# Performance work log

Measured on AMD Instinct MI355X. Metric: run time of the kernel, lower is better.

## Reference

```python
import jax, jax.numpy as jnp
from jax import lax
import numpy as np

N, D, H, ENT = 32768, 16, 128, 50000


def setup_inputs() -> dict:
    key = jax.random.key(0)
    ks = jax.random.split(key, 10)
    s = 0.05  # weight scale to keep tanh/sigmoid in active range
    return {
        "ent_table": jax.random.normal(ks[0], (ENT, H), jnp.float32) * s,
        "op_table": jax.random.normal(ks[1], (5, H), jnp.float32) * s,
        "non_table": jax.random.normal(ks[2], (1, H), jnp.float32) * s,
        "Wm": jax.random.normal(ks[3], (H, 3 * H), jnp.float32) * s,
        "bm": jnp.zeros((H,), jnp.float32),
        "Wg": jax.random.normal(ks[4], (H, 3 * H), jnp.float32) * s,
        "bg": jnp.zeros((H,), jnp.float32),
        "ops_idx": jax.random.randint(ks[5], (N, D), 0, 4, jnp.int32),
        "ents_idx": jax.random.randint(ks[6], (N, D + 1), 0, ENT, jnp.int32),
        "left_idx": jax.random.randint(ks[7], (N,), 0, ENT, jnp.int32),
    }


def reference(ent_table, op_table, non_table, Wm, bm, Wg, bg, ops_idx, ents_idx, left_idx):
    # Merge module (dropout in eval mode = identity):
    #   tanh(Linear([node, t1, t2])) * sigmoid(Linear_g([node, t1, t2]))
    def merge(node, t1, t2):
        x = jnp.concatenate([node, t1, t2], axis=-1)  # [N, 3H]
        return jnp.tanh(x @ Wm.T + bm) * jax.nn.sigmoid(x @ Wg.T + bg)

    op_e = op_table[ops_idx]        # [N, D, H]
    ent_e = ent_table[ents_idx]     # [N, D+1, H]

    # Right-leaning prefix tree: acc starts at deepest entity, merge upward.
    acc0 = ent_e[:, -1]             # [N, H]
    # scan over depth, from innermost (i = D-1) to outermost (i = 0)
    xs = (jnp.flip(op_e, axis=1).transpose(1, 0, 2),          # [D, N, H]
          jnp.flip(ent_e[:, :-1], axis=1).transpose(1, 0, 2))  # [D, N, H]

    def step(acc, inp):
        o, e = inp
        return merge(o, e, acc), None

    acc, _ = lax.scan(step, acc0, xs)

    eq_e = jnp.broadcast_to(op_table[4], acc.shape)  # '=' embedding, [N, H]
    left_e = ent_table[left_idx]                     # [N, H]
    score = merge(eq_e, left_e, acc)                 # [N, H]

    # all_score = cat(per-formula scores, non_embed)  -> [N+1, H]
    return jnp.concatenate([score, non_table], axis=0)
```

## Files before the change

kernel.cpp:

```cpp
#include <hip/hip_runtime.h>
#include <hip/hip_bf16.h>
#include <hip/hip_fp16.h>

#define NROWS 32768
#define HH 128
#define ENTN 50000

typedef _Float16 f16x8 __attribute__((ext_vector_type(8)));
typedef __fp16 fp16x2 __attribute__((ext_vector_type(2)));
typedef float f32x4 __attribute__((ext_vector_type(4)));
typedef float f32x16 __attribute__((ext_vector_type(16)));

#define OFF_PEB 0
#define OFF_WF  25600000
#define OFF_PEF (OFF_WF + 65536)
#define OFF_POPK (OFF_PEF + 65536)

#define KM 2.8853901f
#define KG (-1.4426950f)
#define RSTR 272
#define HALF (32 * RSTR)

#if defined(__has_builtin)
#if __has_builtin(__builtin_amdgcn_exp2f)
#define FEXP2(x) __builtin_amdgcn_exp2f(x)
#endif
#endif
#ifndef FEXP2
__device__ __forceinline__ float __fexp2_asm(float x) {
    float r; asm("v_exp_f32 %0, %1" : "=v"(r) : "v"(x)); return r;
}
#define FEXP2(x) __fexp2_asm(x)
#endif

__device__ __forceinline__ unsigned pk2(float a, float b) {
    fp16x2 h = __builtin_amdgcn_cvt_pkrtz(a, b);
    unsigned u; __builtin_memcpy(&u, &h, 4); return u;
}
__device__ __forceinline__ unsigned pk2rtn(float a, float b) {
    _Float16 lo = (_Float16)a, hi = (_Float16)b;
    unsigned short ul, uh;
    __builtin_memcpy(&ul, &lo, 2); __builtin_memcpy(&uh, &hi, 2);
    return (unsigned)ul | ((unsigned)uh << 16);
}

__global__ void prep_kernel(const float* __restrict__ op_table,
                            const float* __restrict__ non_table,
                            const float* __restrict__ Wm, const float* __restrict__ bm,
                            const float* __restrict__ Wg, const float* __restrict__ bg,
                            char* __restrict__ ws, float* __restrict__ out) {
    int idx = blockIdx.x * blockDim.x + threadIdx.x;
    if (idx < 32768) {
        int e = idx;
        int jj = e & 7, l = (e >> 3) & 63, kt = (e >> 9) & 7, jb = e >> 12;
        int j = jb * 32 + (l & 31);
        int c = j >> 1, p = j & 1;
        int k = kt * 16 + (l >> 5) * 8 + jj;
        const float* Wrow = p ? (Wg + (size_t)c * 384) : (Wm + (size_t)c * 384);
        ((_Float16*)(ws + OFF_WF))[e] = (_Float16)(Wrow[256 + k] * (p ? KG : KM));
    } else if (idx < 65536) {
        int e = idx - 32768;
        int jj = e & 7, l = (e >> 3) & 63, kt = (e >> 9) & 3, jbf = e >> 11;
        int fr = l & 15;
        int j = (jbf >> 1) * 32 + 8 * (fr >> 2) + 4 * (jbf & 1) + (fr & 3);
        int c = j >> 1, p = j & 1;
        int k = kt * 32 + (l >> 4) * 8 + jj;
        const float* Wrow = p ? (Wg + (size_t)c * 384) : (Wm + (size_t)c * 384);
        ((_Float16*)(ws + OFF_PEF))[e] = (_Float16)Wrow[128 + k];
    } else if (idx < 66176) {
        int t2 = idx - 65536;
        int pr = t2 & 1, q = (t2 >> 1) & 3, h = (t2 >> 3) & 1, jb = (t2 >> 4) & 7, o = t2 >> 7;
        int j0 = jb * 32 + 8 * q + 4 * h + 2 * pr;
        int c = j0 >> 1;
        float sm = bm[c], sg = bg[c];
        const float* Wrm = Wm + (size_t)c * 384;
        const float* Wrg = Wg + (size_t)c * 384;
        for (int i = 0; i < 128; ++i) {
            float ov = op_table[o * HH + i];
            sm += ov * Wrm[i];
            sg += ov * Wrg[i];
        }
        ((unsigned*)(ws + OFF_POPK))[t2] = pk2rtn(sm * KM, sg * KG);
    } else if (idx < 66304) {
        int j = idx - 66176;
        out[(size_t)NROWS * HH + j] = non_table[j];
    }
}

__global__ __launch_bounds__(256, 4)
void pe_kernel(const float* __restrict__ ent_table, char* __restrict__ ws) {
    const f16x8* PEF = (const f16x8*)(ws + OFF_PEF);
    char* PEB = ws + OFF_PEB;
    int tid = threadIdx.x, w = tid >> 6, l = tid & 63, lr = l & 15, lg = (l >> 4) & 3;
    int e0 = blockIdx.x * 32;

    f16x8 WB[4][4];
    #pragma unroll
    for (int u = 0; u < 4; ++u)
        #pragma unroll
        for (int kt = 0; kt < 4; ++kt)
            WB[u][kt] = PEF[((4 * w + u) * 4 + kt) * 64 + l];

    f32x4 C[2][4];
    #pragma unroll
    for (int rt = 0; rt < 2; ++rt)
        #pragma unroll
        for (int u = 0; u < 4; ++u) C[rt][u] = (f32x4){0.f, 0.f, 0.f, 0.f};

    #pragma unroll
    for (int kt = 0; kt < 4; ++kt) {
        #pragma unroll
        for (int rt = 0; rt < 2; ++rt) {
            int e = e0 + rt * 16 + lr;
            if (e >= ENTN) e = ENTN - 1;
            const float4* s = (const float4*)(ent_table + (size_t)e * HH + kt * 32 + lg * 8);
            float4 v0 = s[0], v1 = s[1];
            unsigned u4[4] = {pk2(v0.x, v0.y), pk2(v0.z, v0.w),
                              pk2(v1.x, v1.y), pk2(v1.z, v1.w)};
            f16x8 A; __builtin_memcpy(&A, u4, 16);
            #pragma unroll
            for (int u = 0; u < 4; ++u)
                C[rt][u] = __builtin_amdgcn_mfma_f32_16x16x32_f16(WB[u][kt], A, C[rt][u], 0, 0, 0);
        }
    }
    #pragma unroll
    for (int rt = 0; rt < 2; ++rt) {
        int e = e0 + rt * 16 + lr;
        if (e < ENTN) {
            #pragma unroll
            for (int u = 0; u < 4; ++u) {
                int jb2 = 2 * w + (u >> 1);
                uint2 st;
                st.x = pk2(C[rt][u][0] * KM, C[rt][u][1] * KG);
                st.y = pk2(C[rt][u][2] * KM, C[rt][u][3] * KG);
                *(uint2*)(PEB + (size_t)e * 512 + jb2 * 64 + (u & 1) * 32 + lg * 8) = st;
            }
        }
    }
}

__global__ __launch_bounds__(512, 4)
void chain_kernel(const float* __restrict__ ent_table,
                  const int* __restrict__ ops_idx,
                  const int* __restrict__ ents_idx,
                  const int* __restrict__ left_idx,
                  const char* __restrict__ ws, float* __restrict__ out) {
    __shared__ char Abuf[2 * HALF];
    __shared__ unsigned eo[17 * 32];
    __shared__ unsigned popk[640];

    const char* PEBc = ws + OFF_PEB;
    const f16x8* WFp = (const f16x8*)(ws + OFF_WF);
    const unsigned* POPKg = (const unsigned*)(ws + OFF_POPK);

    int tid = threadIdx.x;
    int jb = tid >> 6, l = tid & 63, r = l & 31, h = l >> 5;
    int row0 = blockIdx.x * 32;

    for (int i = tid; i < 544; i += 512) {
        int t = i >> 5, rr = i & 31;
        unsigned e, o;
        if (t < 16) {
            e = ents_idx[(row0 + rr) * 17 + 15 - t];
            o = ops_idx[(row0 + rr) * 16 + 15 - t];
        } else {
            e = left_idx[row0 + rr];
            o = 4;
        }
        eo[i] = (e << 9) | o;
    }
    for (int i = tid; i < 640; i += 512) popk[i] = POPKg[i];

    f16x8 WH[8];
    #pragma unroll
    for (int kt = 0; kt < 8; ++kt)
        WH[kt] = WFp[(jb * 8 + kt) * 64 + l];

    {
        int rr = tid >> 4, sub = tid & 15;
        int e = ents_idx[(row0 + rr) * 17 + 16];
        const float4* src = (const float4*)(ent_table + (size_t)e * HH + sub * 8);
        float4 v0 = src[0], v1 = src[1];
        uint4 d;
        d.x = pk2(v0.x, v0.y); d.y = pk2(v0.z, v0.w);
        d.z = pk2(v1.x, v1.y); d.w = pk2(v1.z, v1.w);
        *(uint4*)(Abuf + rr * RSTR + sub * 16) = d;
    }
    __syncthreads();

    int rb = r * RSTR + h * 16;
    int wb = r * RSTR + jb * 32 + h * 4;
    const char* pebBase = PEBc + jb * 64 + h * 32;
    const char* popkB = (const char*)popk + jb * 64 + h * 32;
    const unsigned* eoB = eo + r;

    unsigned va = eoB[0];
    uint4 pa0 = *(const uint4*)(pebBase + (va & 0xFFFFFE00u));
    uint4 pa1 = *(const uint4*)(pebBase + (va & 0xFFFFFE00u) + 16);

#define DO_STEP(T, RD, WR, FINAL)                                               \
    {                                                                           \
        uint4 npa0, npa1; unsigned nva = 0;                                     \
        if (!(FINAL)) {                                                         \
            nva = eoB[((T) + 1) * 32];                                          \
            npa0 = *(const uint4*)(pebBase + (nva & 0xFFFFFE00u));              \
            npa1 = *(const uint4*)(pebBase + (nva & 0xFFFFFE00u) + 16);         \
        }                                                                       \
        const char* pq = popkB + (va & 7u) * 512;                               \
        uint4 po0 = *(const uint4*)(pq);                                        \
        uint4 po1 = *(const uint4*)(pq + 16);                                   \
        unsigned pe_u[8] = {pa0.x, pa0.y, pa0.z, pa0.w, pa1.x, pa1.y, pa1.z, pa1.w}; \
        unsigned po_u[8] = {po0.x, po0.y, po0.z, po0.w, po1.x, po1.y, po1.z, po1.w}; \
        f32x16 C;                                                               \
        _Pragma("unroll")                                                       \
        for (int q = 0; q < 4; ++q)                                             \
            _Pragma("unroll")                                                   \
            for (int pr = 0; pr < 2; ++pr) {                                    \
                int u = q * 2 + pr;                                             \
                __half2 sa = *(const __half2*)&pe_u[u];                         \
                __half2 sb = *(const __half2*)&po_u[u];                         \
                __half2 s = __hadd2(sa, sb);                                    \
                C[4 * q + 2 * pr] = __low2float(s);                             \
                C[4 * q + 2 * pr + 1] = __high2float(s);                        \
            }                                                                   \
        _Pragma("unroll")                                                       \
        for (int kt = 0; kt < 8; ++kt) {                                        \
            f16x8 A = *(const f16x8*)(Abuf + rb + (RD) + kt * 32);              \
            C = __builtin_amdgcn_mfma_f32_32x32x16_f16(WH[kt], A, C, 0, 0, 0);  \
        }                                                                       \
        _Pragma("unroll")                                                       \
        for (int q = 0; q < 4; ++q) {                                           \
            float ov[2];                                                        \
            _Pragma("unroll")                                                   \
            for (int pr = 0; pr < 2; ++pr) {                                    \
                float m = C[4 * q + 2 * pr];                                    \
                float g = C[4 * q + 2 * pr + 1];                                \
                float em = FEXP2(m), eg = FEXP2(g);                             \
                ov[pr] = (em - 1.f) * __builtin_amdgcn_rcpf((em + 1.f) * (1.f + eg)); \
            }                                                                   \
            if (FINAL) {                                                        \
                *(float2*)(out + (size_t)(row0 + r) * HH + jb * 16 + 4 * q + 2 * h) \
                    = make_float2(ov[0], ov[1]);                                \
            } else {                                                            \
                *(unsigned*)(Abuf + wb + (WR) + q * 8) = pk2(ov[0], ov[1]);     \
            }                                                                   \
        }                                                                       \
        __syncthreads();                                                        \
        if (!(FINAL)) { pa0 = npa0; pa1 = npa1; va = nva; }                     \
    }

    for (int tb = 0; tb < 8; ++tb) {
        int t0 = 2 * tb;
        DO_STEP(t0, 0, HALF, 0)
        DO_STEP(t0 + 1, HALF, 0, 0)
    }
    DO_STEP(16, 0, HALF, 1)
#undef DO_STEP
}

extern "C" void kernel_launch(void* const* d_in, const int* in_sizes, int n_in,
                              void* d_out, int out_size, void* d_ws, size_t ws_size,
                              hipStream_t stream) {
    const float* ent_table = (const float*)d_in[0];
    const float* op_table  = (const float*)d_in[1];
    const float* non_table = (const float*)d_in[2];
    const float* Wm        = (const float*)d_in[3];
    const float* bm        = (const float*)d_in[4];
    const float* Wg        = (const float*)d_in[5];
    const float* bg        = (const float*)d_in[6];
    const int* ops_idx     = (const int*)d_in[7];
    const int* ents_idx    = (const int*)d_in[8];
    const int* left_idx    = (const int*)d_in[9];
    float* out = (float*)d_out;
    char* ws = (char*)d_ws;

    prep_kernel<<<259, 256, 0, stream>>>(op_table, non_table, Wm, bm, Wg, bg, ws, out);
    pe_kernel<<<1563, 256, 0, stream>>>(ent_table, ws);
    chain_kernel<<<NROWS / 32, 512, 0, stream>>>(ent_table, ops_idx, ents_idx,
                                                 left_idx, ws, out);
}
```

Baseline: 103.5 us.

## Process two 32-row tiles per block to amortize weights and barriers

Each chain block now handles 64 rows as two independent 32-row tiles that share the register-resident weight fragments and one barrier per step. This halves the grid size and the per-row cost of loading weights and syncing, and gives each wave two independent MFMA chains to interleave. In exchange, LDS use per block doubles and register pressure rises from the extra prefetched embeddings, which could lower occupancy under the 512x4 launch bounds.

```diff
diff --git a/kernel.cpp b/kernel.cpp
--- a/kernel.cpp
+++ b/kernel.cpp
@@ -20,6 +20,7 @@
 #define KG (-1.4426950f)
 #define RSTR 272
 #define HALF (32 * RSTR)
+#define TILEB (2 * HALF)
 
 #if defined(__has_builtin)
 #if __has_builtin(__builtin_amdgcn_exp2f)
@@ -145,8 +146,8 @@
                   const int* __restrict__ ents_idx,
                   const int* __restrict__ left_idx,
                   const char* __restrict__ ws, float* __restrict__ out) {
-    __shared__ char Abuf[2 * HALF];
-    __shared__ unsigned eo[17 * 32];
+    __shared__ char Abuf[4 * HALF];
+    __shared__ unsigned eo[17 * 64];
     __shared__ unsigned popk[640];
 
     const char* PEBc = ws + OFF_PEB;
@@ -155,10 +156,10 @@
 
     int tid = threadIdx.x;
     int jb = tid >> 6, l = tid & 63, r = l & 31, h = l >> 5;
-    int row0 = blockIdx.x * 32;
-
-    for (int i = tid; i < 544; i += 512) {
-        int t = i >> 5, rr = i & 31;
+    int row0 = blockIdx.x * 64;
+
+    for (int i = tid; i < 17 * 64; i += 512) {
+        int t = i >> 6, rr = i & 63;
         unsigned e, o;
         if (t < 16) {
             e = ents_idx[(row0 + rr) * 17 + 15 - t];
@@ -177,14 +178,18 @@
         WH[kt] = WFp[(jb * 8 + kt) * 64 + l];
 
     {
-        int rr = tid >> 4, sub = tid & 15;
+        int rr = tid >> 3, sub = tid & 7;
         int e = ents_idx[(row0 + rr) * 17 + 16];
-        const float4* src = (const float4*)(ent_table + (size_t)e * HH + sub * 8);
-        float4 v0 = src[0], v1 = src[1];
-        uint4 d;
-        d.x = pk2(v0.x, v0.y); d.y = pk2(v0.z, v0.w);
-        d.z = pk2(v1.x, v1.y); d.w = pk2(v1.z, v1.w);
-        *(uint4*)(Abuf + rr * RSTR + sub * 16) = d;
+        const float4* src = (const float4*)(ent_table + (size_t)e * HH + sub * 16);
+        float4 a = src[0], b = src[1], c2 = src[2], d2 = src[3];
+        uint4 lo, hi;
+        lo.x = pk2(a.x, a.y);  lo.y = pk2(a.z, a.w);
+        lo.z = pk2(b.x, b.y);  lo.w = pk2(b.z, b.w);
+        hi.x = pk2(c2.x, c2.y); hi.y = pk2(c2.z, c2.w);
+        hi.z = pk2(d2.x, d2.y); hi.w = pk2(d2.z, d2.w);
+        char* dst = Abuf + (rr >> 5) * TILEB + (rr & 31) * RSTR + sub * 32;
+        *(uint4*)dst = lo;
+        *(uint4*)(dst + 16) = hi;
     }
     __syncthreads();
 
@@ -194,23 +199,21 @@
     const char* popkB = (const char*)popk + jb * 64 + h * 32;
     const unsigned* eoB = eo + r;
 
-    unsigned va = eoB[0];
-    uint4 pa0 = *(const uint4*)(pebBase + (va & 0xFFFFFE00u));
-    uint4 pa1 = *(const uint4*)(pebBase + (va & 0xFFFFFE00u) + 16);
-
-#define DO_STEP(T, RD, WR, FINAL)                                               \
+    unsigned vaA = eoB[0], vaB = eoB[32];
+    uint4 pa0A = *(const uint4*)(pebBase + (vaA & 0xFFFFFE00u));
+    uint4 pa1A = *(const uint4*)(pebBase + (vaA & 0xFFFFFE00u) + 16);
+    uint4 pa0B = *(const uint4*)(pebBase + (vaB & 0xFFFFFE00u));
+    uint4 pa1B = *(const uint4*)(pebBase + (vaB & 0xFFFFFE00u) + 16);
+
+#define TILE_BODY(VA, PA0, PA1, TOFF, ROWOFF, RD, WR, FINAL)                    \
     {                                                                           \
-        uint4 npa0, npa1; unsigned nva = 0;                                     \
-        if (!(FINAL)) {                                                         \
-            nva = eoB[((T) + 1) * 32];                                          \
-            npa0 = *(const uint4*)(pebBase + (nva & 0xFFFFFE00u));              \
-            npa1 = *(const uint4*)(pebBase + (nva & 0xFFFFFE00u) + 16);         \
-        }                                                                       \
-        const char* pq = popkB + (va & 7u) * 512;                               \
+        const char* pq = popkB + ((VA) & 7u) * 512;                             \
         uint4 po0 = *(const uint4*)(pq);                                        \
         uint4 po1 = *(const uint4*)(pq + 16);                                   \
-        unsigned pe_u[8] = {pa0.x, pa0.y, pa0.z, pa0.w, pa1.x, pa1.y, pa1.z, pa1.w}; \
-        unsigned po_u[8] = {po0.x, po0.y, po0.z, po0.w, po1.x, po1.y, po1.z, po1.w}; \
+        unsigned pe_u[8] = {(PA0).x, (PA0).y, (PA0).z, (PA0).w,                 \
+                            (PA1).x, (PA1).y, (PA1).z, (PA1).w};                \
+        unsigned po_u[8] = {po0.x, po0.y, po0.z, po0.w,                         \
+                            po1.x, po1.y, po1.z, po1.w};                        \
         f32x16 C;                                                               \
         _Pragma("unroll")                                                       \
         for (int q = 0; q < 4; ++q)                                             \
@@ -225,7 +228,7 @@
             }                                                                   \
         _Pragma("unroll")                                                       \
         for (int kt = 0; kt < 8; ++kt) {                                        \
-            f16x8 A = *(const f16x8*)(Abuf + rb + (RD) + kt * 32);              \
+            f16x8 A = *(const f16x8*)(Abuf + (TOFF) + rb + (RD) + kt * 32);     \
             C = __builtin_amdgcn_mfma_f32_32x32x16_f16(WH[kt], A, C, 0, 0, 0);  \
         }                                                                       \
         _Pragma("unroll")                                                       \
@@ -239,14 +242,32 @@
                 ov[pr] = (em - 1.f) * __builtin_amdgcn_rcpf((em + 1.f) * (1.f + eg)); \
             }                                                                   \
             if (FINAL) {                                                        \
-                *(float2*)(out + (size_t)(row0 + r) * HH + jb * 16 + 4 * q + 2 * h) \
-                    = make_float2(ov[0], ov[1]);                                \
+                *(float2*)(out + (size_t)(row0 + (ROWOFF) + r) * HH             \
+                           + jb * 16 + 4 * q + 2 * h) = make_float2(ov[0], ov[1]); \
             } else {                                                            \
-                *(unsigned*)(Abuf + wb + (WR) + q * 8) = pk2(ov[0], ov[1]);     \
+                *(unsigned*)(Abuf + (TOFF) + wb + (WR) + q * 8) = pk2(ov[0], ov[1]); \
             }                                                                   \
         }                                                                       \
+    }
+
+#define DO_STEP(T, RD, WR, FINAL)                                               \
+    {                                                                           \
+        uint4 npa0A, npa1A, npa0B, npa1B; unsigned nvaA = 0, nvaB = 0;          \
+        if (!(FINAL)) {                                                         \
+            nvaA = eoB[((T) + 1) * 64];                                         \
+            nvaB = eoB[((T) + 1) * 64 + 32];                                    \
+            npa0A = *(const uint4*)(pebBase + (nvaA & 0xFFFFFE00u));            \
+            npa1A = *(const uint4*)(pebBase + (nvaA & 0xFFFFFE00u) + 16);       \
+            npa0B = *(const uint4*)(pebBase + (nvaB & 0xFFFFFE00u));            \
+            npa1B = *(const uint4*)(pebBase + (nvaB & 0xFFFFFE00u) + 16);       \
+        }                                                                       \
+        TILE_BODY(vaA, pa0A, pa1A, 0, 0, RD, WR, FINAL)                         \
+        TILE_BODY(vaB, pa0B, pa1B, TILEB, 32, RD, WR, FINAL)                    \
         __syncthreads();                                                        \
-        if (!(FINAL)) { pa0 = npa0; pa1 = npa1; va = nva; }                     \
+        if (!(FINAL)) {                                                         \
+            pa0A = npa0A; pa1A = npa1A; vaA = nvaA;                             \
+            pa0B = npa0B; pa1B = npa1B; vaB = nvaB;                             \
+        }                                                                       \
     }
 
     for (int tb = 0; tb < 8; ++tb) {
@@ -256,6 +277,7 @@
     }
     DO_STEP(16, 0, HALF, 1)
 #undef DO_STEP
+#undef TILE_BODY
 }
 
 extern "C" void kernel_launch(void* const* d_in, const int* in_sizes, int n_in,
@@ -276,6 +298,6 @@
 
     prep_kernel<<<259, 256, 0, stream>>>(op_table, non_table, Wm, bm, Wg, bg, ws, out);
     pe_kernel<<<1563, 256, 0, stream>>>(ent_table, ws);
-    chain_kernel<<<NROWS / 32, 512, 0, stream>>>(ent_table, ops_idx, ents_idx,
+    chain_kernel<<<NROWS / 64, 512, 0, stream>>>(ent_table, ops_idx, ents_idx,
                                                  left_idx, ws, out);
 }
```

After: 99.79 us, median of 2. -3.6%, faster.
